# Kernel tuning notes

Measured on AMD Instinct MI355X. Metric: run time of the kernel, lower is better.

Reference implementation:

```python
import jax, jax.numpy as jnp
import numpy as np

NUM_BLOCKS = 10  # labels 1..10; label 0 = background
EPS = 1e-6


def setup_inputs() -> dict:
    key = jax.random.key(0)
    k1, k2, k3 = jax.random.split(key, 3)
    shape = (8, 128, 128, 128)
    inp = jax.random.uniform(k1, shape, dtype=jnp.float32)
    tgt = jax.random.uniform(k2, shape, dtype=jnp.float32)
    blk = jax.random.randint(k3, shape, 0, NUM_BLOCKS + 1, dtype=jnp.int32)
    return {"input": inp, "target": tgt, "block": blk}


def _dice_from_sums(intersect, input_area, target_area):
    # intersect/areas: [B, NUM_BLOCKS]; faithful to cal_dice_loss per block.
    denom = input_area + target_area + 2.0 * EPS
    batch_loss = 1.0 - 2.0 * intersect / denom          # [B, NUM_BLOCKS]
    batch_loss = jnp.where(target_area == 0, 0.0, batch_loss)
    valid = jnp.sum(target_area != 0, axis=0).astype(batch_loss.dtype)  # [NUM_BLOCKS]
    return jnp.sum(batch_loss, axis=0) / jnp.maximum(valid, 1.0)        # [NUM_BLOCKS]


def reference(input, target, block):
    B = input.shape[0]
    x = input.reshape(B, -1)
    t = target.reshape(B, -1)
    s = block.reshape(B, -1)

    # One fused pass: per-batch segmented sums over block ids 0..NUM_BLOCKS.
    seg = jax.vmap(lambda v, ids: jax.ops.segment_sum(v, ids, num_segments=NUM_BLOCKS + 1))
    intersect = seg(x * t, s)[:, 1:]   # [B, 10] sum(input*target) within each block
    input_area = seg(x, s)[:, 1:]      # [B, 10]
    target_area = seg(t, s)[:, 1:]     # [B, 10]

    loss_per_block = _dice_from_sums(intersect, input_area, target_area)  # [10]

    # block_tmp.max() != 0  <=>  label b+1 appears anywhere in the tensor
    counts = jnp.sum(s[..., None] == jnp.arange(1, NUM_BLOCKS + 1), axis=(0, 1))
    present = counts > 0                                                   # [10]
    num = jnp.sum(present).astype(loss_per_block.dtype)
    loss = jnp.sum(jnp.where(present, loss_per_block, 0.0)) / num
    return (loss, 0)
```

## Files before the change

### kernel.cpp

```cpp
#include <hip/hip_runtime.h>

#define NB 10
#define BATCH 8
#define EPSF 1e-6f

constexpr int ELEMS_PER_BATCH = 128 * 128 * 128;
constexpr int VEC_PER_BATCH   = ELEMS_PER_BATCH / 4;
constexpr int THREADS         = 256;
constexpr int VPT             = 8;
constexpr int SLICE_VEC       = THREADS * VPT;
constexpr int BLOCKS_PER_BATCH = 64;
constexpr int SLICES_PER_BLOCK = VEC_PER_BATCH / (SLICE_VEC * BLOCKS_PER_BATCH);
constexpr int GRID            = BLOCKS_PER_BATCH * BATCH;

constexpr int REC = 32;

__global__ __launch_bounds__(THREADS)
__attribute__((amdgpu_waves_per_eu(2, 2)))
void dice_partial(const float* __restrict__ x,
                  const float* __restrict__ t,
                  const int*   __restrict__ s,
                  float* __restrict__ ws)
{
    const int tid   = threadIdx.x;
    const int batch = blockIdx.x >> 6;
    const int sub   = blockIdx.x & 63;

    float aI[NB], aX[NB], aT[NB];
#pragma unroll
    for (int k = 0; k < NB; ++k) { aI[k] = 0.f; aX[k] = 0.f; aT[k] = 0.f; }
    unsigned bits = 0;

#define DO_ELEM(xe, te, se)                                     \
    do {                                                        \
        const float _x = (xe), _t = (te);                       \
        const int   _s = (se);                                  \
        const float _p = _x * _t;                               \
        bits |= (1u << _s);                                     \
        _Pragma("unroll")                                       \
        for (int k = 0; k < NB; ++k) {                          \
            const float m = (_s == k + 1) ? 1.0f : 0.0f;        \
            aI[k] = fmaf(m, _p, aI[k]);                         \
            aX[k] = fmaf(m, _x, aX[k]);                         \
            aT[k] = fmaf(m, _t, aT[k]);                         \
        }                                                       \
    } while (0)

#pragma unroll 1
    for (int j = 0; j < SLICES_PER_BLOCK; ++j) {
        const long long base = (long long)batch * VEC_PER_BATCH
                             + (long long)(sub + BLOCKS_PER_BATCH * j) * SLICE_VEC;
        const float4* x4 = reinterpret_cast<const float4*>(x) + base;
        const float4* t4 = reinterpret_cast<const float4*>(t) + base;
        const int4*   s4 = reinterpret_cast<const int4*>(s)   + base;

        float4 xv[VPT], tv[VPT]; int4 sv[VPT];
#pragma unroll
        for (int i = 0; i < VPT; ++i) {
            const int idx = i * THREADS + tid;
            xv[i] = x4[idx];
            tv[i] = t4[idx];
            sv[i] = s4[idx];
        }
        asm volatile("" ::: "memory");

#pragma unroll
        for (int i = 0; i < VPT; ++i) {
            DO_ELEM(xv[i].x, tv[i].x, sv[i].x);
            DO_ELEM(xv[i].y, tv[i].y, sv[i].y);
            DO_ELEM(xv[i].z, tv[i].z, sv[i].z);
            DO_ELEM(xv[i].w, tv[i].w, sv[i].w);
        }
    }
#undef DO_ELEM

#pragma unroll
    for (int k = 0; k < NB; ++k) {
#pragma unroll
        for (int off = 32; off > 0; off >>= 1) {
            aI[k] += __shfl_xor(aI[k], off);
            aX[k] += __shfl_xor(aX[k], off);
            aT[k] += __shfl_xor(aT[k], off);
        }
    }
#pragma unroll
    for (int off = 32; off > 0; off >>= 1)
        bits |= (unsigned)__shfl_xor((int)bits, off);

    __shared__ float    wsum[4][32];
    __shared__ unsigned wb[4];
    const int wave = tid >> 6, lane = tid & 63;
    if (lane < NB) {
        wsum[wave][lane]          = aI[lane];
        wsum[wave][NB + lane]     = aX[lane];
        wsum[wave][2 * NB + lane] = aT[lane];
    }
    if (lane == 0) wb[wave] = bits;
    __syncthreads();

    if (tid < 3 * NB) {
        const float v = wsum[0][tid] + wsum[1][tid] + wsum[2][tid] + wsum[3][tid];
        ws[blockIdx.x * REC + tid] = v;
    }
    if (tid == 0)
        ((unsigned*)ws)[blockIdx.x * REC + 30] = wb[0] | wb[1] | wb[2] | wb[3];
}

__global__ void dice_final(const float* __restrict__ ws, float* __restrict__ out)
{
    const int tid = threadIdx.x;
    __shared__ float    sAll[BATCH][3 * NB];
    __shared__ unsigned um[THREADS];

    if (tid < BATCH * 3 * NB) {
        const int batch = tid / (3 * NB);
        const int idx   = tid % (3 * NB);
        float v = 0.0f;
        for (int j = 0; j < BLOCKS_PER_BATCH; ++j)
            v += ws[(batch * BLOCKS_PER_BATCH + j) * REC + idx];
        sAll[batch][idx] = v;
    }

    unsigned m = 0;
#pragma unroll
    for (int j = 0; j < GRID / THREADS; ++j)
        m |= ((const unsigned*)ws)[(tid * (GRID / THREADS) + j) * REC + 30];
    um[tid] = m;
    __syncthreads();
    for (int st = THREADS / 2; st > 0; st >>= 1) {
        if (tid < st) um[tid] |= um[tid + st];
        __syncthreads();
    }
    const unsigned mask = um[0];

    if (tid < 64) {
        float lpb = 0.0f, pres = 0.0f;
        if (tid < NB) {
            float sum_loss = 0.0f, valid = 0.0f;
            for (int b = 0; b < BATCH; ++b) {
                const float I = sAll[b][tid];
                const float X = sAll[b][NB + tid];
                const float T = sAll[b][2 * NB + tid];
                const float denom = X + T + 2.0f * EPSF;
                float bl = 1.0f - 2.0f * I / denom;
                if (T == 0.0f) bl = 0.0f; else valid += 1.0f;
                sum_loss += bl;
            }
            lpb  = sum_loss / fmaxf(valid, 1.0f);
            pres = ((mask >> (tid + 1)) & 1u) ? 1.0f : 0.0f;
        }
        float num = pres;
        float ls  = (pres > 0.0f) ? lpb : 0.0f;
#pragma unroll
        for (int off = 32; off > 0; off >>= 1) {
            num += __shfl_down(num, off);
            ls  += __shfl_down(ls,  off);
        }
        if (tid == 0) {
            out[0] = ls / num;
            out[1] = 0.0f;
        }
    }
}

extern "C" void kernel_launch(void* const* d_in, const int* in_sizes, int n_in,
                              void* d_out, int out_size, void* d_ws, size_t ws_size,
                              hipStream_t stream)
{
    const float* x = (const float*)d_in[0];
    const float* t = (const float*)d_in[1];
    const int*   s = (const int*)d_in[2];
    float* out = (float*)d_out;
    float* ws  = (float*)d_ws;

    dice_partial<<<GRID, THREADS, 0, stream>>>(x, t, s, ws);
    dice_final<<<1, THREADS, 0, stream>>>(ws, out);
}
```

Baseline: 50.61 us.

## Stream inputs through LDS with async global_load_lds multi-stage pipeline per wave

Replaces register-staged batched float4 loads with per-wave asynchronous global-to-LDS DMA (global_load_lds) in a 4-buffer ring with 3 loads in flight, using explicit vmcnt waits. Each wave now owns a contiguous 2048-vector chunk instead of block-strided slices, and the waves_per_eu constraint is dropped. The aim is to overlap memory latency with the segmented-sum arithmetic and reduce register pressure. It adds LDS usage, hand-tuned waitcnt assumptions, and relies on LDS reads being correctly ordered after the DMA without explicit barriers.

```diff
diff --git a/kernel.cpp b/kernel.cpp
--- a/kernel.cpp
+++ b/kernel.cpp
@@ -4,27 +4,40 @@
 #define BATCH 8
 #define EPSF 1e-6f
 
-constexpr int ELEMS_PER_BATCH = 128 * 128 * 128;
-constexpr int VEC_PER_BATCH   = ELEMS_PER_BATCH / 4;
-constexpr int THREADS         = 256;
-constexpr int VPT             = 8;
-constexpr int SLICE_VEC       = THREADS * VPT;
+constexpr int THREADS        = 256;
+constexpr int VEC_PER_BATCH  = (128 * 128 * 128) / 4;
 constexpr int BLOCKS_PER_BATCH = 64;
-constexpr int SLICES_PER_BLOCK = VEC_PER_BATCH / (SLICE_VEC * BLOCKS_PER_BATCH);
-constexpr int GRID            = BLOCKS_PER_BATCH * BATCH;
-
+constexpr int GRID           = BLOCKS_PER_BATCH * BATCH;
+constexpr int WAVE_VEC       = 2048;
+constexpr int STAGES         = WAVE_VEC / 64;
 constexpr int REC = 32;
 
+__device__ __forceinline__ void dma16(const void* g, void* l) {
+    __builtin_amdgcn_global_load_lds(
+        (const __attribute__((address_space(1))) void*)g,
+        (__attribute__((address_space(3))) void*)l, 16, 0, 0);
+}
+
 __global__ __launch_bounds__(THREADS)
-__attribute__((amdgpu_waves_per_eu(2, 2)))
 void dice_partial(const float* __restrict__ x,
                   const float* __restrict__ t,
                   const int*   __restrict__ s,
                   float* __restrict__ ws)
 {
-    const int tid   = threadIdx.x;
+    __shared__ float4 lx[4][4][64];
+    __shared__ float4 lt[4][4][64];
+    __shared__ int4   lsb[4][4][64];
+
+    const int tid  = threadIdx.x;
+    const int wave = tid >> 6, lane = tid & 63;
     const int batch = blockIdx.x >> 6;
     const int sub   = blockIdx.x & 63;
+    const long long chunk = (long long)batch * VEC_PER_BATCH
+                          + (long long)(sub * 4 + wave) * WAVE_VEC;
+
+    const float4* gx = (const float4*)x + chunk + lane;
+    const float4* gt = (const float4*)t + chunk + lane;
+    const int4*   gs = (const int4*)s  + chunk + lane;
 
     float aI[NB], aX[NB], aT[NB];
 #pragma unroll
@@ -46,31 +59,39 @@
         }                                                       \
     } while (0)
 
+#pragma unroll
+    for (int i = 0; i < 3; ++i) {
+        dma16(gx + i * 64, &lx[wave][i][0]);
+        dma16(gt + i * 64, &lt[wave][i][0]);
+        dma16(gs + i * 64, &lsb[wave][i][0]);
+    }
+    const float4* px = gx + 3 * 64;
+    const float4* pt = gt + 3 * 64;
+    const int4*   ps = gs + 3 * 64;
+
 #pragma unroll 1
-    for (int j = 0; j < SLICES_PER_BLOCK; ++j) {
-        const long long base = (long long)batch * VEC_PER_BATCH
-                             + (long long)(sub + BLOCKS_PER_BATCH * j) * SLICE_VEC;
-        const float4* x4 = reinterpret_cast<const float4*>(x) + base;
-        const float4* t4 = reinterpret_cast<const float4*>(t) + base;
-        const int4*   s4 = reinterpret_cast<const int4*>(s)   + base;
+    for (int i = 0; i < STAGES; ++i) {
+        if (i <= STAGES - 3)      asm volatile("s_waitcnt vmcnt(6)" ::: "memory");
+        else if (i == STAGES - 2) asm volatile("s_waitcnt vmcnt(3)" ::: "memory");
+        else                      asm volatile("s_waitcnt vmcnt(0)" ::: "memory");
+        __builtin_amdgcn_sched_barrier(0);
 
-        float4 xv[VPT], tv[VPT]; int4 sv[VPT];
-#pragma unroll
-        for (int i = 0; i < VPT; ++i) {
-            const int idx = i * THREADS + tid;
-            xv[i] = x4[idx];
-            tv[i] = t4[idx];
-            sv[i] = s4[idx];
+        if (i < STAGES - 3) {
+            const int nb = (i + 3) & 3;
+            dma16(px, &lx[wave][nb][0]);
+            dma16(pt, &lt[wave][nb][0]);
+            dma16(ps, &lsb[wave][nb][0]);
+            px += 64; pt += 64; ps += 64;
         }
-        asm volatile("" ::: "memory");
 
-#pragma unroll
-        for (int i = 0; i < VPT; ++i) {
-            DO_ELEM(xv[i].x, tv[i].x, sv[i].x);
-            DO_ELEM(xv[i].y, tv[i].y, sv[i].y);
-            DO_ELEM(xv[i].z, tv[i].z, sv[i].z);
-            DO_ELEM(xv[i].w, tv[i].w, sv[i].w);
-        }
+        const int b = i & 3;
+        const float4 xv = lx[wave][b][lane];
+        const float4 tv = lt[wave][b][lane];
+        const int4   sv = lsb[wave][b][lane];
+        DO_ELEM(xv.x, tv.x, sv.x);
+        DO_ELEM(xv.y, tv.y, sv.y);
+        DO_ELEM(xv.z, tv.z, sv.z);
+        DO_ELEM(xv.w, tv.w, sv.w);
     }
 #undef DO_ELEM
 
@@ -89,7 +110,6 @@
 
     __shared__ float    wsum[4][32];
     __shared__ unsigned wb[4];
-    const int wave = tid >> 6, lane = tid & 63;
     if (lane < NB) {
         wsum[wave][lane]          = aI[lane];
         wsum[wave][NB + lane]     = aX[lane];
```

Result: faster. 45.66 us (median of 2 runs) (-9.8%).
